# Optimization experiments

Hardware: AMD Instinct MI355X
Metric: run time of the kernel (lower is better)

The kernel has to match this reference:

```python
import jax, jax.numpy as jnp
import numpy as np

A = -4.0
a = 1.0
b = 1.0


def setup_inputs() -> dict:
    key = jax.random.key(0)
    k1, k2 = jax.random.split(key)
    B, C = 16384, 10000
    outputs = jax.random.normal(k1, (B, C), dtype=jnp.float32)
    targets = jax.random.randint(k2, (B,), 0, C, dtype=jnp.int64)
    return {"outputs": outputs, "targets": targets}


def reference(outputs, targets):
    # x = log_softmax(outputs, axis=1); y = softmax
    logp = jax.nn.log_softmax(outputs, axis=1)          # [B, C]
    p = jnp.exp(logp)                                    # [B, C]
    B = outputs.shape[0]
    idx = jnp.arange(B)
    logp_t = logp[idx, targets]                          # gathered log-prob of target
    p_t = p[idx, targets]                                # gathered prob of target
    # ce = -(1/B) * sum_i logp[i, t_i]
    ce = -jnp.mean(logp_t)
    # ces = (A/B) * sum_i (p[i, t_i] - sum_j p[i, j])
    ces = (jnp.sum(p_t) - jnp.sum(p)) * (A / B)
    return a * ce + b * ces
```

## Files before the change

### kernel.cpp

```cpp
#include <hip/hip_runtime.h>

#define B_DIM 16384
#define C_DIM 10000
#define C_VEC (C_DIM / 4)
#define A_CONST (-4.0f)

__device__ inline void combine(float& m, float& s, float mo, float so) {
    float mn = fmaxf(m, mo);
    s = s * __expf(m - mn) + so * __expf(mo - mn);
    m = mn;
}

__global__ __launch_bounds__(256) void ces_row_kernel(
        const float* __restrict__ x,
        const int* __restrict__ tgt,
        float* __restrict__ row_out) {
    const int row = blockIdx.x;
    const float* xr = x + (size_t)row * C_DIM;
    const float4* xv = reinterpret_cast<const float4*>(xr);
    const int tid = threadIdx.x;

    float m = -3.0e38f;
    float s = 0.0f;
    for (int j = tid; j < C_VEC; j += 256) {
        float4 v = xv[j];
        float m4 = fmaxf(fmaxf(v.x, v.y), fmaxf(v.z, v.w));
        float mn = fmaxf(m, m4);
        s = s * __expf(m - mn)
          + __expf(v.x - mn) + __expf(v.y - mn)
          + __expf(v.z - mn) + __expf(v.w - mn);
        m = mn;
    }

    #pragma unroll
    for (int off = 32; off >= 1; off >>= 1) {
        float mo = __shfl_xor(m, off);
        float so = __shfl_xor(s, off);
        combine(m, s, mo, so);
    }

    __shared__ float sm[4], ss[4];
    const int wave = tid >> 6;
    if ((tid & 63) == 0) { sm[wave] = m; ss[wave] = s; }
    __syncthreads();

    if (tid == 0) {
        m = sm[0]; s = ss[0];
        #pragma unroll
        for (int w = 1; w < 4; ++w) combine(m, s, sm[w], ss[w]);

        const int t = tgt[row];
        const float xt = xr[t];
        const float logs = __logf(s);
        const float neg_logp_t = m + logs - xt;
        const float p_t = __expf(xt - m) / s;
        row_out[row] = (1.0f / B_DIM) * neg_logp_t
                     + (A_CONST / B_DIM) * (p_t - 1.0f);
    }
}

__global__ __launch_bounds__(1024) void ces_reduce_kernel(
        const float* __restrict__ row_out,
        float* __restrict__ out) {
    __shared__ float sm[16];
    const int tid = threadIdx.x;
    float acc = 0.0f;
    #pragma unroll
    for (int j = tid; j < B_DIM; j += 1024) acc += row_out[j];
    #pragma unroll
    for (int off = 32; off >= 1; off >>= 1) acc += __shfl_xor(acc, off);
    if ((tid & 63) == 0) sm[tid >> 6] = acc;
    __syncthreads();
    if (tid == 0) {
        float r = 0.0f;
        #pragma unroll
        for (int w = 0; w < 16; ++w) r += sm[w];
        out[0] = r;
    }
}

extern "C" void kernel_launch(void* const* d_in, const int* in_sizes, int n_in,
                              void* d_out, int out_size, void* d_ws, size_t ws_size,
                              hipStream_t stream) {
    const float* outputs = (const float*)d_in[0];
    const int*   targets = (const int*)d_in[1];
    float* row_out = (float*)d_ws;
    float* out = (float*)d_out;

    ces_row_kernel<<<B_DIM, 256, 0, stream>>>(outputs, targets, row_out);
    ces_reduce_kernel<<<1, 1024, 0, stream>>>(row_out, out);
}
```

Before: 118.8 us.

## Assign one wave per row with grid-stride loop and per-wave partial sums

Replaces the one-block-per-row kernel with a persistent grid of 2048 blocks. Each 64-lane wave walks rows in a grid-stride loop, reduces max and sum-exp with shuffles only, and accumulates the per-row loss contribution in a register. This removes the shared-memory exchange and __syncthreads per row and shrinks the second-stage reduction from 16384 to 8192 partials. In exchange each lane now loops about 40 float4 loads per row instead of about 10, which leaves less memory-level parallelism per wave.

```diff
diff --git a/kernel.cpp b/kernel.cpp
--- a/kernel.cpp
+++ b/kernel.cpp
@@ -5,68 +5,62 @@
 #define C_VEC (C_DIM / 4)
 #define A_CONST (-4.0f)
 
+#define NBLK 2048
+#define WAVES_PER_BLK 4
+#define NWAVES (NBLK * WAVES_PER_BLK)
+
 __device__ inline void combine(float& m, float& s, float mo, float so) {
     float mn = fmaxf(m, mo);
     s = s * __expf(m - mn) + so * __expf(mo - mn);
     m = mn;
 }
 
-__global__ __launch_bounds__(256) void ces_row_kernel(
+__global__ __launch_bounds__(256) void ces_rows_kernel(
         const float* __restrict__ x,
         const int* __restrict__ tgt,
-        float* __restrict__ row_out) {
-    const int row = blockIdx.x;
-    const float* xr = x + (size_t)row * C_DIM;
-    const float4* xv = reinterpret_cast<const float4*>(xr);
-    const int tid = threadIdx.x;
+        float* __restrict__ partial) {
+    const int lane = threadIdx.x & 63;
+    const int wid  = blockIdx.x * WAVES_PER_BLK + (threadIdx.x >> 6);
 
-    float m = -3.0e38f;
-    float s = 0.0f;
-    for (int j = tid; j < C_VEC; j += 256) {
-        float4 v = xv[j];
-        float m4 = fmaxf(fmaxf(v.x, v.y), fmaxf(v.z, v.w));
-        float mn = fmaxf(m, m4);
-        s = s * __expf(m - mn)
-          + __expf(v.x - mn) + __expf(v.y - mn)
-          + __expf(v.z - mn) + __expf(v.w - mn);
-        m = mn;
+    float acc = 0.0f;
+    for (int row = wid; row < B_DIM; row += NWAVES) {
+        const float* xr = x + (size_t)row * C_DIM;
+        const float4* xv = reinterpret_cast<const float4*>(xr);
+
+        float m = -3.0e38f;
+        float s = 0.0f;
+        for (int j = lane; j < C_VEC; j += 64) {
+            float4 v = xv[j];
+            float m4 = fmaxf(fmaxf(v.x, v.y), fmaxf(v.z, v.w));
+            float mn = fmaxf(m, m4);
+            s = s * __expf(m - mn)
+              + __expf(v.x - mn) + __expf(v.y - mn)
+              + __expf(v.z - mn) + __expf(v.w - mn);
+            m = mn;
+        }
+
+        #pragma unroll
+        for (int off = 32; off >= 1; off >>= 1) {
+            combine(m, s, __shfl_xor(m, off), __shfl_xor(s, off));
+        }
+
+        const float xt = xr[tgt[row]];
+        const float neg_logp_t = m + __logf(s) - xt;
+        const float p_t = __expf(xt - m) / s;
+        acc += (1.0f / B_DIM) * neg_logp_t
+             + (A_CONST / B_DIM) * (p_t - 1.0f);
     }
-
-    #pragma unroll
-    for (int off = 32; off >= 1; off >>= 1) {
-        float mo = __shfl_xor(m, off);
-        float so = __shfl_xor(s, off);
-        combine(m, s, mo, so);
-    }
-
-    __shared__ float sm[4], ss[4];
-    const int wave = tid >> 6;
-    if ((tid & 63) == 0) { sm[wave] = m; ss[wave] = s; }
-    __syncthreads();
-
-    if (tid == 0) {
-        m = sm[0]; s = ss[0];
-        #pragma unroll
-        for (int w = 1; w < 4; ++w) combine(m, s, sm[w], ss[w]);
-
-        const int t = tgt[row];
-        const float xt = xr[t];
-        const float logs = __logf(s);
-        const float neg_logp_t = m + logs - xt;
-        const float p_t = __expf(xt - m) / s;
-        row_out[row] = (1.0f / B_DIM) * neg_logp_t
-                     + (A_CONST / B_DIM) * (p_t - 1.0f);
-    }
+    if (lane == 0) partial[wid] = acc;
 }
 
 __global__ __launch_bounds__(1024) void ces_reduce_kernel(
-        const float* __restrict__ row_out,
+        const float* __restrict__ partial,
         float* __restrict__ out) {
     __shared__ float sm[16];
     const int tid = threadIdx.x;
     float acc = 0.0f;
     #pragma unroll
-    for (int j = tid; j < B_DIM; j += 1024) acc += row_out[j];
+    for (int k = 0; k < NWAVES / 1024; ++k) acc += partial[tid + k * 1024];
     #pragma unroll
     for (int off = 32; off >= 1; off >>= 1) acc += __shfl_xor(acc, off);
     if ((tid & 63) == 0) sm[tid >> 6] = acc;
@@ -84,9 +78,9 @@
                               hipStream_t stream) {
     const float* outputs = (const float*)d_in[0];
     const int*   targets = (const int*)d_in[1];
-    float* row_out = (float*)d_ws;
+    float* partial = (float*)d_ws;
     float* out = (float*)d_out;
 
-    ces_row_kernel<<<B_DIM, 256, 0, stream>>>(outputs, targets, row_out);
-    ces_reduce_kernel<<<1, 1024, 0, stream>>>(row_out, out);
+    ces_rows_kernel<<<NBLK, 256, 0, stream>>>(outputs, targets, partial);
+    ces_reduce_kernel<<<1, 1024, 0, stream>>>(partial, out);
 }
```

Result: no change. 118.9 us (+0.1%).
